# Optimization experiments

Hardware: AMD Instinct MI355X
Metric: run time of the kernel (lower is better)

## Reference

```python
import jax, jax.numpy as jnp
import numpy as np

N_QUBITS = 10
N_QLAYERS = 4
INV_SQRT2 = 1.0 / np.sqrt(2.0)


def setup_inputs() -> dict:
    key = jax.random.key(0)
    k1, k2 = jax.random.split(key)
    x = jax.random.normal(k1, (16, 256, 2 * N_QUBITS), dtype=jnp.float32)
    weights = jax.random.uniform(k2, (N_QLAYERS, N_QUBITS, 3), dtype=jnp.float32,
                                 minval=-np.pi, maxval=np.pi)
    return {"x": x, "weights": weights}


def _ry_mat(t):
    # t: scalar or (B,) -> (...,2,2) complex64 rotation about Y
    c = jnp.cos(t * 0.5)
    s = jnp.sin(t * 0.5)
    row0 = jnp.stack([c, -s], axis=-1)
    row1 = jnp.stack([s, c], axis=-1)
    return jnp.stack([row0, row1], axis=-2).astype(jnp.complex64)


def _rz_mat(p):
    # t: scalar or (B,) -> (...,2,2) complex64 diag(e^{-ip/2}, e^{+ip/2})
    e = jnp.exp(-0.5j * p.astype(jnp.complex64))
    z = jnp.zeros_like(e)
    row0 = jnp.stack([e, z], axis=-1)
    row1 = jnp.stack([z, jnp.conj(e)], axis=-1)
    return jnp.stack([row0, row1], axis=-2)


def _apply_1q(state, U, wire):
    # state: (B, 2,...,2); U: (2,2) shared or (B,2,2) per-sample
    ax = wire + 1
    s = jnp.moveaxis(state, ax, -1)
    if U.ndim == 3:
        s = jnp.einsum('bij,b...j->b...i', U, s)
    else:
        s = jnp.einsum('ij,...j->...i', U, s)
    return jnp.moveaxis(s, -1, ax)


def _apply_cnot(state, ctrl, tgt):
    a, b = ctrl + 1, tgt + 1
    s0 = jax.lax.index_in_dim(state, 0, axis=a, keepdims=True)
    s1 = jax.lax.index_in_dim(state, 1, axis=a, keepdims=True)
    s1 = jnp.flip(s1, axis=b)  # X on target within control=1 block
    return jnp.concatenate([s0, s1], axis=a)


def _circuit(x_flat, weights):
    n = N_QUBITS
    Bf = x_flat.shape[0]
    theta = jnp.pi * (x_flat[:, :n] + 1.0) * 0.5
    phi = jnp.pi * (x_flat[:, n:2 * n] + 1.0) * 0.5
    H = jnp.array([[1.0, 1.0], [1.0, -1.0]], dtype=jnp.complex64) * INV_SQRT2

    # |0...0> batched statevector: (Bf, 2, ..., 2)
    state = jnp.zeros((Bf, 2 ** n), dtype=jnp.complex64).at[:, 0].set(1.0)
    state = state.reshape((Bf,) + (2,) * n)

    # encoding layer
    for i in range(n):
        state = _apply_1q(state, H, i)
        state = _apply_1q(state, _ry_mat(theta[:, i]), i)
        state = _apply_1q(state, _rz_mat(phi[:, i]), i)

    # variational layers
    for layer in range(N_QLAYERS):
        for i in range(n):
            state = _apply_1q(state, _rz_mat(weights[layer, i, 0]), i)
            state = _apply_1q(state, _ry_mat(weights[layer, i, 1]), i)
            state = _apply_1q(state, _rz_mat(weights[layer, i, 2]), i)
        off = 1 if layer % 2 == 0 else n // 2
        for i in range(n):
            state = _apply_cnot(state, i, (i + off) % n)

    # <Z_i> = sum |amp|^2 * (+1 if qubit i = 0 else -1)
    probs = state.real ** 2 + state.imag ** 2
    zs = []
    for i in range(n):
        p = jnp.moveaxis(probs, i + 1, -1).reshape(Bf, -1, 2)
        zs.append(p[..., 0].sum(-1) - p[..., 1].sum(-1))
    return jnp.stack(zs, axis=-1)  # (Bf, n_qubits)


def reference(x, weights):
    B, L, _ = x.shape
    out = _circuit(x.reshape(-1, 2 * N_QUBITS), weights)
    return out.reshape(B, L, N_QUBITS)
```

## Files before the change

### kernel.cpp

```cpp
#include <hip/hip_runtime.h>
#include <math.h>

#define NQ 10
#define NLAYERS 4
#define NGATES (NLAYERS * NQ)

typedef float v2f __attribute__((ext_vector_type(2)));
typedef float v4f __attribute__((ext_vector_type(4)));

__device__ __forceinline__ v2f mk2(float a, float b) { v2f r; r.x = a; r.y = b; return r; }

__device__ __forceinline__ v2f cmul_m(v4f m, v2f s) {
    v2f r = m.xy * s;
    return __builtin_elementwise_fma(m.zw, s.yx, r);
}
__device__ __forceinline__ v2f cfma_m(v2f acc, v4f m, v2f s) {
    acc = __builtin_elementwise_fma(m.xy, s, acc);
    acc = __builtin_elementwise_fma(m.zw, s.yx, acc);
    return acc;
}
__device__ __forceinline__ v2f cmul(v2f a, v2f b) {
    v2f r = a.xx * b;
    return __builtin_elementwise_fma(mk2(-a.y, a.y), b.yx, r);
}
__device__ __forceinline__ v4f pack_u(float re, float im) {
    v4f m; m.x = re; m.y = re; m.z = -im; m.w = im; return m;
}

__host__ __device__ constexpr int pxor1(int v) {
    int y = v; y ^= y >> 1; y ^= y >> 2; y ^= y >> 4; y ^= y >> 8;
    return (y & 0x1FF) | (((y ^ (v >> 9)) & 1) << 9);
}
__host__ __device__ constexpr int pxor5(int v) {
    int lo = v & 31, hi = (v >> 5) & 31;
    return (lo << 5) | (lo ^ hi);
}

__device__ __forceinline__ void apply_gate(v2f* st, const v4f* __restrict__ M, int b) {
    v4f m0 = M[0], m1 = M[1], m2 = M[2], m3 = M[3];
    #pragma unroll
    for (int g = 0; g < 16; ++g) {
        int r0 = ((g >> b) << (b + 1)) | (g & ((1 << b) - 1));
        int r1 = r0 | (1 << b);
        v2f s0v = st[r0], s1v = st[r1];
        v2f n0 = cmul_m(m0, s0v); n0 = cfma_m(n0, m1, s1v);
        v2f n1 = cmul_m(m2, s0v); n1 = cfma_m(n1, m3, s1v);
        st[r0] = n0; st[r1] = n1;
    }
}

__device__ __forceinline__ void load_contig(v2f* st, const v2f* scratch, int lane) {
    const v4f* rp = (const v4f*)(scratch + 34 * lane);
    #pragma unroll
    for (int k = 0; k < 16; ++k) { v4f t = rp[k]; st[2 * k] = t.xy; st[2 * k + 1] = t.zw; }
}

__global__ __launch_bounds__(64) void qsim_kernel(const float* __restrict__ x,
                                                  const float* __restrict__ w,
                                                  float* __restrict__ out)
{
    __shared__ __align__(16) v2f scratch[2176];
    __shared__ __align__(16) v4f matsL[NGATES * 4];
    __shared__ __align__(16) v2f encf[2][NQ][2];

    const int lane = threadIdx.x;
    const int s = lane >> 5, sl = lane & 31;
    const long sample = 2L * blockIdx.x + s;

    if (lane < NGATES) {
        float w0 = w[lane * 3 + 0], w1 = w[lane * 3 + 1], w2 = w[lane * 3 + 2];
        float hs = 0.5f * (w0 + w2), hd = 0.5f * (w0 - w2), hy = 0.5f * w1;
        float cy, sy, cs, ss, cd, sd;
        sincosf(hy, &sy, &cy);
        sincosf(hs, &ss, &cs);
        sincosf(hd, &sd, &cd);
        matsL[lane * 4 + 0] = pack_u( cy * cs, -cy * ss);
        matsL[lane * 4 + 1] = pack_u(-sy * cd, -sy * sd);
        matsL[lane * 4 + 2] = pack_u( sy * cd, -sy * sd);
        matsL[lane * 4 + 3] = pack_u( cy * cs,  cy * ss);
    }
    __syncthreads();

    if (sl < NQ) {
        const float* xs = x + sample * (2 * NQ);
        float th = 0.7853981633974483f * (xs[sl] + 1.0f);
        float ph = 0.7853981633974483f * (xs[NQ + sl] + 1.0f);
        float cy, sy, cp, sp;
        sincosf(th, &sy, &cy);
        sincosf(ph, &sp, &cp);
        const float inv = 0.7071067811865476f;
        float a = (cy - sy) * inv, b = (cy + sy) * inv;
        v2f f0 = mk2(cp * a, -sp * a);
        v2f f1 = mk2(cp * b,  sp * b);
        v4f M0 = matsL[sl * 4 + 0], M1 = matsL[sl * 4 + 1];
        v4f M2 = matsL[sl * 4 + 2], M3 = matsL[sl * 4 + 3];
        encf[s][sl][0] = cfma_m(cmul_m(M0, f0), M1, f1);
        encf[s][sl][1] = cfma_m(cmul_m(M2, f0), M3, f1);
    }
    __syncthreads();

    v2f st[32];
    {
        v2f P = encf[s][5][(sl >> 4) & 1];
        P = cmul(P, encf[s][6][(sl >> 3) & 1]);
        P = cmul(P, encf[s][7][(sl >> 2) & 1]);
        P = cmul(P, encf[s][8][(sl >> 1) & 1]);
        P = cmul(P, encf[s][9][sl & 1]);
        v2f q01[4], q23[4], q234[8], Pq[4];
        #pragma unroll
        for (int a2 = 0; a2 < 4; ++a2) {
            q01[a2] = cmul(encf[s][0][(a2 >> 1) & 1], encf[s][1][a2 & 1]);
            q23[a2] = cmul(encf[s][2][(a2 >> 1) & 1], encf[s][3][a2 & 1]);
        }
        #pragma unroll
        for (int b2 = 0; b2 < 8; ++b2)
            q234[b2] = cmul(q23[b2 >> 1], encf[s][4][b2 & 1]);
        #pragma unroll
        for (int a2 = 0; a2 < 4; ++a2) Pq[a2] = cmul(P, q01[a2]);
        #pragma unroll
        for (int r = 0; r < 32; ++r)
            st[r] = cmul(Pq[r >> 3], q234[r & 7]);
    }

    const int jb1 = pxor1(sl), jb5 = pxor5(sl);

    #pragma unroll
    for (int r = 0; r < 32; ++r) {
        const int j = pxor1(r << 5) ^ jb1;
        scratch[1088 * s + 34 * (j >> 5) + (j & 31)] = st[r];
    }
    __syncthreads();
    load_contig(st, scratch, lane);

    #pragma unroll
    for (int l = 1; l < NLAYERS; ++l) {
        #pragma unroll
        for (int q = 5; q <= 9; ++q)
            apply_gate(st, matsL + (l * NQ + q) * 4, 9 - q);

        __syncthreads();
        {
            v2f* wp = scratch + 1088 * s + sl;
            #pragma unroll
            for (int r = 0; r < 32; ++r) wp[34 * r] = st[r];
        }
        __syncthreads();
        load_contig(st, scratch, lane);

        #pragma unroll
        for (int q = 0; q <= 4; ++q)
            apply_gate(st, matsL + (l * NQ + q) * 4, 4 - q);

        if (l < NLAYERS - 1) {
            __syncthreads();
            #pragma unroll
            for (int r = 0; r < 32; ++r) {
                const int jc = (l & 1) ? pxor5(r << 5) : pxor1(r << 5);
                const int j = jc ^ ((l & 1) ? jb5 : jb1);
                scratch[1088 * s + 34 * (j >> 5) + (j & 31)] = st[r];
            }
            __syncthreads();
            load_contig(st, scratch, lane);
        }
    }

    {
        float p[32];
        #pragma unroll
        for (int r = 0; r < 32; ++r) {
            v2f a = st[r];
            v2f sq = a * a;
            p[r] = sq.x + sq.y;
        }
        float t0 = 0.f, t1 = 0.f, t2 = 0.f, t3 = 0.f, t4 = 0.f;
        float s0a[16], s1a[8], s2a[4], s3a[2];
        #pragma unroll
        for (int k = 0; k < 16; ++k) { s0a[k] = p[2*k] + p[2*k+1]; t0 += p[2*k] - p[2*k+1]; }
        #pragma unroll
        for (int k = 0; k < 8; ++k)  { s1a[k] = s0a[2*k] + s0a[2*k+1]; t1 += s0a[2*k] - s0a[2*k+1]; }
        #pragma unroll
        for (int k = 0; k < 4; ++k)  { s2a[k] = s1a[2*k] + s1a[2*k+1]; t2 += s1a[2*k] - s1a[2*k+1]; }
        #pragma unroll
        for (int k = 0; k < 2; ++k)  { s3a[k] = s2a[2*k] + s2a[2*k+1]; t3 += s2a[2*k] - s2a[2*k+1]; }
        float S = s3a[0] + s3a[1];   t4 = s3a[0] - s3a[1];

        float acc[NQ];
        #pragma unroll
        for (int q = 0; q < 5; ++q)
            acc[q] = ((sl >> (4 - q)) & 1) ? -S : S;
        acc[5] = ((sl >> 4) & 1) ? -t4 : t4;
        acc[6] = ((sl >> 3) & 1) ? -t3 : t3;
        acc[7] = ((sl >> 2) & 1) ? -t2 : t2;
        acc[8] = ((sl >> 1) & 1) ? -t1 : t1;
        acc[9] = (sl & 1)        ? -t0 : t0;

        #pragma unroll
        for (int q = 0; q < NQ; ++q) {
            #pragma unroll
            for (int o = 16; o >= 1; o >>= 1)
                acc[q] += __shfl_xor(acc[q], o);
        }
        float v = acc[0];
        #pragma unroll
        for (int q = 1; q < NQ; ++q) v = (sl == q) ? acc[q] : v;
        if (sl < NQ)
            out[sample * NQ + sl] = v;
    }
}

extern "C" void kernel_launch(void* const* d_in, const int* in_sizes, int n_in,
                              void* d_out, int out_size, void* d_ws, size_t ws_size,
                              hipStream_t stream) {
    const float* x = (const float*)d_in[0];
    const float* w = (const float*)d_in[1];
    float* out = (float*)d_out;
    const int n_samples = in_sizes[0] / (2 * NQ);
    qsim_kernel<<<n_samples / 2, 64, 0, stream>>>(x, w, out);
}
```

Before: 77.23 us.

## Spread each sample's statevector across a full 64-lane wave with shuffle gates

Each block now simulates one sample using all 64 lanes, so each lane holds 16 amplitudes instead of 32 and register pressure drops (launch bounds now request 4 waves). Two qubits per layer are applied through cross-lane shuffles instead of in-register pairs. Unitary storage is halved by exploiting SU(2) structure, the shared-memory transposes use an XOR swizzle instead of padding, and the final reduction becomes a butterfly of Walsh-style shuffles. The cost is more shuffle traffic and twice as many blocks.

Result: slower. 83.28 us (+7.8%).

```diff
diff --git a/kernel.cpp b/kernel.cpp
--- a/kernel.cpp
+++ b/kernel.cpp
@@ -19,6 +19,15 @@
     acc = __builtin_elementwise_fma(m.zw, s.yx, acc);
     return acc;
 }
+__device__ __forceinline__ v2f cmul_mc(v4f m, v2f s) {
+    v2f r = m.xy * s;
+    return __builtin_elementwise_fma(-m.zw, s.yx, r);
+}
+__device__ __forceinline__ v2f cfms_mc(v2f acc, v4f m, v2f s) {
+    acc = __builtin_elementwise_fma(-m.xy, s, acc);
+    acc = __builtin_elementwise_fma(m.zw, s.yx, acc);
+    return acc;
+}
 __device__ __forceinline__ v2f cmul(v2f a, v2f b) {
     v2f r = a.xx * b;
     return __builtin_elementwise_fma(mk2(-a.y, a.y), b.yx, r);
@@ -36,55 +45,73 @@
     return (lo << 5) | (lo ^ hi);
 }
 
-__device__ __forceinline__ void apply_gate(v2f* st, const v4f* __restrict__ M, int b) {
-    v4f m0 = M[0], m1 = M[1], m2 = M[2], m3 = M[3];
-    #pragma unroll
-    for (int g = 0; g < 16; ++g) {
+__device__ __forceinline__ void apply_gate16(v2f* st, const v4f* __restrict__ M, int b) {
+    v4f m0 = M[0], m1 = M[1];
+    #pragma unroll
+    for (int g = 0; g < 8; ++g) {
         int r0 = ((g >> b) << (b + 1)) | (g & ((1 << b) - 1));
         int r1 = r0 | (1 << b);
-        v2f s0v = st[r0], s1v = st[r1];
-        v2f n0 = cmul_m(m0, s0v); n0 = cfma_m(n0, m1, s1v);
-        v2f n1 = cmul_m(m2, s0v); n1 = cfma_m(n1, m3, s1v);
-        st[r0] = n0; st[r1] = n1;
-    }
-}
-
-__device__ __forceinline__ void load_contig(v2f* st, const v2f* scratch, int lane) {
-    const v4f* rp = (const v4f*)(scratch + 34 * lane);
-    #pragma unroll
-    for (int k = 0; k < 16; ++k) { v4f t = rp[k]; st[2 * k] = t.xy; st[2 * k + 1] = t.zw; }
-}
-
-__global__ __launch_bounds__(64) void qsim_kernel(const float* __restrict__ x,
-                                                  const float* __restrict__ w,
-                                                  float* __restrict__ out)
+        v2f s0 = st[r0], s1 = st[r1];
+        st[r0] = cfma_m(cmul_m(m0, s0), m1, s1);
+        st[r1] = cfms_mc(cmul_mc(m0, s1), m1, s0);
+    }
+}
+
+__device__ __forceinline__ v2f shflx2(v2f v, int m) {
+    v2f r;
+    r.x = __shfl_xor(v.x, m, 64);
+    r.y = __shfl_xor(v.y, m, 64);
+    return r;
+}
+
+__device__ __forceinline__ void apply_gate_lane(v2f* st, const v4f* __restrict__ M, int m, int lane) {
+    v4f m0 = M[0], m1 = M[1];
+    v4f mA = m0, mB = m1;
+    if (lane & m) { mA.z = -mA.z; mA.w = -mA.w; mB.x = -mB.x; mB.y = -mB.y; }
+    #pragma unroll
+    for (int r = 0; r < 16; ++r) {
+        v2f mine = st[r];
+        v2f th = shflx2(mine, m);
+        st[r] = cfma_m(cmul_m(mA, mine), mB, th);
+    }
+}
+
+__device__ __forceinline__ void read_row(v2f* st, const v2f* scratch, int lane) {
+    const int e = (lane & 7) << 1;
+    const v2f* row = scratch + lane * 16;
+    #pragma unroll
+    for (int h = 0; h < 8; ++h) {
+        v4f t = *(const v4f*)(row + ((2 * h) ^ e));
+        st[2 * h]     = t.xy;
+        st[2 * h + 1] = t.zw;
+    }
+}
+
+__global__ __launch_bounds__(64, 4) void qsim_kernel(const float* __restrict__ x,
+                                                     const float* __restrict__ w,
+                                                     float* __restrict__ out)
 {
-    __shared__ __align__(16) v2f scratch[2176];
-    __shared__ __align__(16) v4f matsL[NGATES * 4];
-    __shared__ __align__(16) v2f encf[2][NQ][2];
+    __shared__ __align__(16) v2f scratch[1024];
+    __shared__ __align__(16) v4f matsL[NGATES * 2];
+    __shared__ __align__(16) v2f encf[NQ][2];
 
     const int lane = threadIdx.x;
-    const int s = lane >> 5, sl = lane & 31;
-    const long sample = 2L * blockIdx.x + s;
+    const long sample = blockIdx.x;
 
     if (lane < NGATES) {
-        float w0 = w[lane * 3 + 0], w1 = w[lane * 3 + 1], w2 = w[lane * 3 + 2];
-        float hs = 0.5f * (w0 + w2), hd = 0.5f * (w0 - w2), hy = 0.5f * w1;
+        float w0 = w[lane*3+0], w1 = w[lane*3+1], w2 = w[lane*3+2];
+        float hs = 0.5f*(w0+w2), hd = 0.5f*(w0-w2), hy = 0.5f*w1;
         float cy, sy, cs, ss, cd, sd;
         sincosf(hy, &sy, &cy);
         sincosf(hs, &ss, &cs);
         sincosf(hd, &sd, &cd);
-        matsL[lane * 4 + 0] = pack_u( cy * cs, -cy * ss);
-        matsL[lane * 4 + 1] = pack_u(-sy * cd, -sy * sd);
-        matsL[lane * 4 + 2] = pack_u( sy * cd, -sy * sd);
-        matsL[lane * 4 + 3] = pack_u( cy * cs,  cy * ss);
-    }
-    __syncthreads();
-
-    if (sl < NQ) {
+        matsL[lane*2+0] = pack_u( cy*cs, -cy*ss);
+        matsL[lane*2+1] = pack_u(-sy*cd, -sy*sd);
+    }
+    if (lane < NQ) {
         const float* xs = x + sample * (2 * NQ);
-        float th = 0.7853981633974483f * (xs[sl] + 1.0f);
-        float ph = 0.7853981633974483f * (xs[NQ + sl] + 1.0f);
+        float th = 0.7853981633974483f * (xs[lane] + 1.0f);
+        float ph = 0.7853981633974483f * (xs[NQ + lane] + 1.0f);
         float cy, sy, cp, sp;
         sincosf(th, &sy, &cy);
         sincosf(ph, &sp, &cp);
@@ -92,119 +119,121 @@
         float a = (cy - sy) * inv, b = (cy + sy) * inv;
         v2f f0 = mk2(cp * a, -sp * a);
         v2f f1 = mk2(cp * b,  sp * b);
-        v4f M0 = matsL[sl * 4 + 0], M1 = matsL[sl * 4 + 1];
-        v4f M2 = matsL[sl * 4 + 2], M3 = matsL[sl * 4 + 3];
-        encf[s][sl][0] = cfma_m(cmul_m(M0, f0), M1, f1);
-        encf[s][sl][1] = cfma_m(cmul_m(M2, f0), M3, f1);
+        v4f M0 = matsL[lane*2+0], M1 = matsL[lane*2+1];
+        encf[lane][0] = cfma_m(cmul_m(M0, f0), M1, f1);
+        encf[lane][1] = cfms_mc(cmul_mc(M0, f1), M1, f0);
     }
     __syncthreads();
 
-    v2f st[32];
+    v2f st[16];
     {
-        v2f P = encf[s][5][(sl >> 4) & 1];
-        P = cmul(P, encf[s][6][(sl >> 3) & 1]);
-        P = cmul(P, encf[s][7][(sl >> 2) & 1]);
-        P = cmul(P, encf[s][8][(sl >> 1) & 1]);
-        P = cmul(P, encf[s][9][sl & 1]);
-        v2f q01[4], q23[4], q234[8], Pq[4];
+        v2f L = cmul(encf[4][(lane >> 5) & 1], encf[5][(lane >> 4) & 1]);
+        L = cmul(L, encf[6][(lane >> 3) & 1]);
+        L = cmul(L, encf[7][(lane >> 2) & 1]);
+        L = cmul(L, encf[8][(lane >> 1) & 1]);
+        L = cmul(L, encf[9][lane & 1]);
+        v2f hi2[4], lo2[4], Lh[4];
         #pragma unroll
         for (int a2 = 0; a2 < 4; ++a2) {
-            q01[a2] = cmul(encf[s][0][(a2 >> 1) & 1], encf[s][1][a2 & 1]);
-            q23[a2] = cmul(encf[s][2][(a2 >> 1) & 1], encf[s][3][a2 & 1]);
-        }
-        #pragma unroll
-        for (int b2 = 0; b2 < 8; ++b2)
-            q234[b2] = cmul(q23[b2 >> 1], encf[s][4][b2 & 1]);
-        #pragma unroll
-        for (int a2 = 0; a2 < 4; ++a2) Pq[a2] = cmul(P, q01[a2]);
-        #pragma unroll
-        for (int r = 0; r < 32; ++r)
-            st[r] = cmul(Pq[r >> 3], q234[r & 7]);
-    }
-
-    const int jb1 = pxor1(sl), jb5 = pxor5(sl);
-
-    #pragma unroll
-    for (int r = 0; r < 32; ++r) {
-        const int j = pxor1(r << 5) ^ jb1;
-        scratch[1088 * s + 34 * (j >> 5) + (j & 31)] = st[r];
-    }
+            hi2[a2] = cmul(encf[0][(a2 >> 1) & 1], encf[1][a2 & 1]);
+            lo2[a2] = cmul(encf[2][(a2 >> 1) & 1], encf[3][a2 & 1]);
+        }
+        #pragma unroll
+        for (int a2 = 0; a2 < 4; ++a2) Lh[a2] = cmul(L, hi2[a2]);
+        #pragma unroll
+        for (int r = 0; r < 16; ++r)
+            st[r] = cmul(Lh[r >> 2], lo2[r & 3]);
+    }
+
+    const int jb1 = pxor1(lane), jb5 = pxor5(lane);
+
     __syncthreads();
-    load_contig(st, scratch, lane);
+    #pragma unroll
+    for (int r = 0; r < 16; ++r) {
+        const int jc = pxor1(r << 6);
+        const int jp = jc ^ jb1;
+        const int row = jp >> 4;
+        scratch[(row << 4) + ((jp & 15) ^ ((row & 7) << 1))] = st[r];
+    }
+    __syncthreads();
+    read_row(st, scratch, lane);
 
     #pragma unroll
     for (int l = 1; l < NLAYERS; ++l) {
-        #pragma unroll
-        for (int q = 5; q <= 9; ++q)
-            apply_gate(st, matsL + (l * NQ + q) * 4, 9 - q);
+        const v4f* Ml = matsL + l * NQ * 2;
+        apply_gate16(st, Ml + 6*2, 3);
+        apply_gate16(st, Ml + 7*2, 2);
+        apply_gate16(st, Ml + 8*2, 1);
+        apply_gate16(st, Ml + 9*2, 0);
+        apply_gate_lane(st, Ml + 4*2, 2, lane);
+        apply_gate_lane(st, Ml + 5*2, 1, lane);
 
         __syncthreads();
         {
-            v2f* wp = scratch + 1088 * s + sl;
+            const int b0 = (lane & 3) << 8;
+            const int cc = lane >> 2;
             #pragma unroll
-            for (int r = 0; r < 32; ++r) wp[34 * r] = st[r];
+            for (int r = 0; r < 16; ++r)
+                scratch[b0 + (r << 4) + (cc ^ ((r & 7) << 1))] = st[r];
         }
         __syncthreads();
-        load_contig(st, scratch, lane);
-
-        #pragma unroll
-        for (int q = 0; q <= 4; ++q)
-            apply_gate(st, matsL + (l * NQ + q) * 4, 4 - q);
+        read_row(st, scratch, lane);
+
+        apply_gate16(st, Ml + 0*2, 3);
+        apply_gate16(st, Ml + 1*2, 2);
+        apply_gate16(st, Ml + 2*2, 1);
+        apply_gate16(st, Ml + 3*2, 0);
 
         if (l < NLAYERS - 1) {
             __syncthreads();
+            const int jb = (l & 1) ? jb5 : jb1;
             #pragma unroll
-            for (int r = 0; r < 32; ++r) {
-                const int jc = (l & 1) ? pxor5(r << 5) : pxor1(r << 5);
-                const int j = jc ^ ((l & 1) ? jb5 : jb1);
-                scratch[1088 * s + 34 * (j >> 5) + (j & 31)] = st[r];
+            for (int r = 0; r < 16; ++r) {
+                const int jc = (l & 1) ? pxor5(r << 6) : pxor1(r << 6);
+                const int jp = jc ^ jb;
+                const int row = jp >> 4;
+                scratch[(row << 4) + ((jp & 15) ^ ((row & 7) << 1))] = st[r];
             }
             __syncthreads();
-            load_contig(st, scratch, lane);
+            read_row(st, scratch, lane);
         }
     }
 
     {
-        float p[32];
-        #pragma unroll
-        for (int r = 0; r < 32; ++r) {
-            v2f a = st[r];
-            v2f sq = a * a;
-            p[r] = sq.x + sq.y;
-        }
-        float t0 = 0.f, t1 = 0.f, t2 = 0.f, t3 = 0.f, t4 = 0.f;
-        float s0a[16], s1a[8], s2a[4], s3a[2];
-        #pragma unroll
-        for (int k = 0; k < 16; ++k) { s0a[k] = p[2*k] + p[2*k+1]; t0 += p[2*k] - p[2*k+1]; }
-        #pragma unroll
-        for (int k = 0; k < 8; ++k)  { s1a[k] = s0a[2*k] + s0a[2*k+1]; t1 += s0a[2*k] - s0a[2*k+1]; }
-        #pragma unroll
-        for (int k = 0; k < 4; ++k)  { s2a[k] = s1a[2*k] + s1a[2*k+1]; t2 += s1a[2*k] - s1a[2*k+1]; }
-        #pragma unroll
-        for (int k = 0; k < 2; ++k)  { s3a[k] = s2a[2*k] + s2a[2*k+1]; t3 += s2a[2*k] - s2a[2*k+1]; }
-        float S = s3a[0] + s3a[1];   t4 = s3a[0] - s3a[1];
-
-        float acc[NQ];
-        #pragma unroll
-        for (int q = 0; q < 5; ++q)
-            acc[q] = ((sl >> (4 - q)) & 1) ? -S : S;
-        acc[5] = ((sl >> 4) & 1) ? -t4 : t4;
-        acc[6] = ((sl >> 3) & 1) ? -t3 : t3;
-        acc[7] = ((sl >> 2) & 1) ? -t2 : t2;
-        acc[8] = ((sl >> 1) & 1) ? -t1 : t1;
-        acc[9] = (sl & 1)        ? -t0 : t0;
-
-        #pragma unroll
-        for (int q = 0; q < NQ; ++q) {
-            #pragma unroll
-            for (int o = 16; o >= 1; o >>= 1)
-                acc[q] += __shfl_xor(acc[q], o);
-        }
-        float v = acc[0];
-        #pragma unroll
-        for (int q = 1; q < NQ; ++q) v = (sl == q) ? acc[q] : v;
-        if (sl < NQ)
-            out[sample * NQ + sl] = v;
+        float p[16];
+        #pragma unroll
+        for (int r = 0; r < 16; ++r) {
+            v2f a = st[r]; v2f q2 = a * a; p[r] = q2.x + q2.y;
+        }
+        float s0[8], s1[4], s2[2];
+        float tb0 = 0.f, tb1 = 0.f, tb2, tb3, S;
+        #pragma unroll
+        for (int k = 0; k < 8; ++k) { s0[k] = p[2*k] + p[2*k+1]; tb0 += p[2*k] - p[2*k+1]; }
+        #pragma unroll
+        for (int k = 0; k < 4; ++k) { s1[k] = s0[2*k] + s0[2*k+1]; tb1 += s0[2*k] - s0[2*k+1]; }
+        #pragma unroll
+        for (int k = 0; k < 2; ++k) { s2[k] = s1[2*k] + s1[2*k+1]; }
+        tb2 = (s1[0] - s1[1]) + (s1[2] - s1[3]);
+        S   = s2[0] + s2[1];
+        tb3 = s2[0] - s2[1];
+
+        float wS = S, w0t = tb0, w1t = tb1, w2t = tb2, w3t = tb3;
+        #pragma unroll
+        for (int m = 1; m < 64; m <<= 1) {
+            float t;
+            t = __shfl_xor(wS,  m, 64); wS  = (lane & m) ? (t - wS)  : (wS  + t);
+            t = __shfl_xor(w0t, m, 64); w0t = (lane & m) ? (t - w0t) : (w0t + t);
+            t = __shfl_xor(w1t, m, 64); w1t = (lane & m) ? (t - w1t) : (w1t + t);
+            t = __shfl_xor(w2t, m, 64); w2t = (lane & m) ? (t - w2t) : (w2t + t);
+            t = __shfl_xor(w3t, m, 64); w3t = (lane & m) ? (t - w3t) : (w3t + t);
+        }
+        float* ob = out + sample * NQ;
+        if (lane == 16)      { ob[0] = wS; ob[5] = w3t; }
+        else if (lane == 8)  { ob[1] = wS; ob[6] = w2t; }
+        else if (lane == 4)  { ob[2] = wS; ob[7] = w1t; }
+        else if (lane == 2)  { ob[3] = wS; ob[8] = w0t; }
+        else if (lane == 1)  { ob[4] = wS; }
+        else if (lane == 33) { ob[9] = wS; }
     }
 }
 
@@ -215,5 +244,5 @@
     const float* w = (const float*)d_in[1];
     float* out = (float*)d_out;
     const int n_samples = in_sizes[0] / (2 * NQ);
-    qsim_kernel<<<n_samples / 2, 64, 0, stream>>>(x, w, out);
-}
+    qsim_kernel<<<n_samples, 64, 0, stream>>>(x, w, out);
+}
```

## Build initial state directly in permuted layout and compress gate matrices

Applied to the files above, without the earlier changes.

Builds the product-state encoding directly in the register layout that follows the first CNOT permutation, which removes one LDS write/sync/read round trip. Each SU(2) gate is now stored as a single v4f (a, b) instead of four packed v4f, which cuts LDS reads per gate, and the packed-vector complex math is replaced with scalar fmaf chains. The risk is a change in instruction count and VALU packing, since scalar fma may not use the v_pk_fma path.

Result: slower. 84.81 us (+9.8%).

```diff
diff --git a/kernel.cpp b/kernel.cpp
--- a/kernel.cpp
+++ b/kernel.cpp
@@ -10,21 +10,18 @@
 
 __device__ __forceinline__ v2f mk2(float a, float b) { v2f r; r.x = a; r.y = b; return r; }
 
-__device__ __forceinline__ v2f cmul_m(v4f m, v2f s) {
-    v2f r = m.xy * s;
-    return __builtin_elementwise_fma(m.zw, s.yx, r);
-}
-__device__ __forceinline__ v2f cfma_m(v2f acc, v4f m, v2f s) {
-    acc = __builtin_elementwise_fma(m.xy, s, acc);
-    acc = __builtin_elementwise_fma(m.zw, s.yx, acc);
-    return acc;
-}
-__device__ __forceinline__ v2f cmul(v2f a, v2f b) {
-    v2f r = a.xx * b;
-    return __builtin_elementwise_fma(mk2(-a.y, a.y), b.yx, r);
-}
-__device__ __forceinline__ v4f pack_u(float re, float im) {
-    v4f m; m.x = re; m.y = re; m.z = -im; m.w = im; return m;
+__device__ __forceinline__ v2f cmulS(v2f a, v2f b) {
+    return mk2(fmaf(a.x, b.x, -(a.y * b.y)), fmaf(a.x, b.y, a.y * b.x));
+}
+__device__ __forceinline__ v2f grow0(v4f m, v2f s0, v2f s1) {
+    float re = fmaf(m.x, s0.x, fmaf(-m.y, s0.y, fmaf(m.z, s1.x, -(m.w * s1.y))));
+    float im = fmaf(m.x, s0.y, fmaf( m.y, s0.x, fmaf(m.z, s1.y,   m.w * s1.x)));
+    return mk2(re, im);
+}
+__device__ __forceinline__ v2f grow1(v4f m, v2f s0, v2f s1) {
+    float re = fmaf(-m.z, s0.x, fmaf(-m.w, s0.y, fmaf(m.x, s1.x,   m.y * s1.y)));
+    float im = fmaf( m.w, s0.x, fmaf(-m.z, s0.y, fmaf(m.x, s1.y, -(m.y * s1.x))));
+    return mk2(re, im);
 }
 
 __host__ __device__ constexpr int pxor1(int v) {
@@ -36,16 +33,14 @@
     return (lo << 5) | (lo ^ hi);
 }
 
-__device__ __forceinline__ void apply_gate(v2f* st, const v4f* __restrict__ M, int b) {
-    v4f m0 = M[0], m1 = M[1], m2 = M[2], m3 = M[3];
+__device__ __forceinline__ void apply_gate(v2f* st, v4f m, int b) {
     #pragma unroll
     for (int g = 0; g < 16; ++g) {
         int r0 = ((g >> b) << (b + 1)) | (g & ((1 << b) - 1));
         int r1 = r0 | (1 << b);
-        v2f s0v = st[r0], s1v = st[r1];
-        v2f n0 = cmul_m(m0, s0v); n0 = cfma_m(n0, m1, s1v);
-        v2f n1 = cmul_m(m2, s0v); n1 = cfma_m(n1, m3, s1v);
-        st[r0] = n0; st[r1] = n1;
+        v2f s0 = st[r0], s1 = st[r1];
+        st[r0] = grow0(m, s0, s1);
+        st[r1] = grow1(m, s0, s1);
     }
 }
 
@@ -60,7 +55,7 @@
                                                   float* __restrict__ out)
 {
     __shared__ __align__(16) v2f scratch[2176];
-    __shared__ __align__(16) v4f matsL[NGATES * 4];
+    __shared__ __align__(16) v4f matsL[NGATES];
     __shared__ __align__(16) v2f encf[2][NQ][2];
 
     const int lane = threadIdx.x;
@@ -74,10 +69,8 @@
         sincosf(hy, &sy, &cy);
         sincosf(hs, &ss, &cs);
         sincosf(hd, &sd, &cd);
-        matsL[lane * 4 + 0] = pack_u( cy * cs, -cy * ss);
-        matsL[lane * 4 + 1] = pack_u(-sy * cd, -sy * sd);
-        matsL[lane * 4 + 2] = pack_u( sy * cd, -sy * sd);
-        matsL[lane * 4 + 3] = pack_u( cy * cs,  cy * ss);
+        v4f m; m.x = cy * cs; m.y = -cy * ss; m.z = -sy * cd; m.w = -sy * sd;
+        matsL[lane] = m;
     }
     __syncthreads();
 
@@ -92,51 +85,49 @@
         float a = (cy - sy) * inv, b = (cy + sy) * inv;
         v2f f0 = mk2(cp * a, -sp * a);
         v2f f1 = mk2(cp * b,  sp * b);
-        v4f M0 = matsL[sl * 4 + 0], M1 = matsL[sl * 4 + 1];
-        v4f M2 = matsL[sl * 4 + 2], M3 = matsL[sl * 4 + 3];
-        encf[s][sl][0] = cfma_m(cmul_m(M0, f0), M1, f1);
-        encf[s][sl][1] = cfma_m(cmul_m(M2, f0), M3, f1);
+        v4f m = matsL[sl];
+        encf[s][sl][0] = grow0(m, f0, f1);
+        encf[s][sl][1] = grow1(m, f0, f1);
     }
     __syncthreads();
 
     v2f st[32];
     {
-        v2f P = encf[s][5][(sl >> 4) & 1];
-        P = cmul(P, encf[s][6][(sl >> 3) & 1]);
-        P = cmul(P, encf[s][7][(sl >> 2) & 1]);
-        P = cmul(P, encf[s][8][(sl >> 1) & 1]);
-        P = cmul(P, encf[s][9][sl & 1]);
-        v2f q01[4], q23[4], q234[8], Pq[4];
-        #pragma unroll
-        for (int a2 = 0; a2 < 4; ++a2) {
-            q01[a2] = cmul(encf[s][0][(a2 >> 1) & 1], encf[s][1][a2 & 1]);
-            q23[a2] = cmul(encf[s][2][(a2 >> 1) & 1], encf[s][3][a2 & 1]);
-        }
-        #pragma unroll
-        for (int b2 = 0; b2 < 8; ++b2)
-            q234[b2] = cmul(q23[b2 >> 1], encf[s][4][b2 & 1]);
-        #pragma unroll
-        for (int a2 = 0; a2 < 4; ++a2) Pq[a2] = cmul(P, q01[a2]);
-        #pragma unroll
-        for (int r = 0; r < 32; ++r)
-            st[r] = cmul(Pq[r >> 3], q234[r & 7]);
+        v2f Lc = cmulS(encf[s][2][((sl >> 2) ^ (sl >> 3)) & 1],
+                 cmulS(encf[s][3][((sl >> 1) ^ (sl >> 2)) & 1],
+                       encf[s][4][(sl ^ (sl >> 1)) & 1]));
+        v2f g5s0 = encf[s][5][sl & 1];
+        v2f g5s1 = encf[s][5][(sl & 1) ^ 1];
+        const int l4 = (sl >> 4) & 1, l34 = ((sl >> 3) ^ (sl >> 4)) & 1;
+        v2f h0 = cmulS(encf[s][0][l4],     encf[s][1][l34]);
+        v2f h1 = cmulS(encf[s][0][l4 ^ 1], encf[s][1][l34 ^ 1]);
+        v2f k4[4];
+        k4[0] = cmulS(encf[s][9][0], h0);
+        k4[1] = cmulS(encf[s][9][1], h1);
+        k4[2] = cmulS(encf[s][9][1], h0);
+        k4[3] = cmulS(encf[s][9][0], h1);
+        v2f Av[2], Bv[4], Cv[8], Dv[16];
+        Av[0] = cmulS(Lc, g5s0); Av[1] = cmulS(Lc, g5s1);
+        #pragma unroll
+        for (int i = 0; i < 4; ++i)  Bv[i] = cmulS(Av[i >> 1], encf[s][6][((i >> 1) ^ i) & 1]);
+        #pragma unroll
+        for (int i = 0; i < 8; ++i)  Cv[i] = cmulS(Bv[i >> 1], encf[s][7][((i >> 1) ^ i) & 1]);
+        #pragma unroll
+        for (int i = 0; i < 16; ++i) Dv[i] = cmulS(Cv[i >> 1], encf[s][8][((i >> 1) ^ i) & 1]);
+        #pragma unroll
+        for (int r = 0; r < 32; ++r) st[r] = cmulS(Dv[r >> 1], k4[r & 3]);
     }
 
     const int jb1 = pxor1(sl), jb5 = pxor5(sl);
-
-    #pragma unroll
-    for (int r = 0; r < 32; ++r) {
-        const int j = pxor1(r << 5) ^ jb1;
-        scratch[1088 * s + 34 * (j >> 5) + (j & 31)] = st[r];
-    }
-    __syncthreads();
-    load_contig(st, scratch, lane);
 
     #pragma unroll
     for (int l = 1; l < NLAYERS; ++l) {
-        #pragma unroll
-        for (int q = 5; q <= 9; ++q)
-            apply_gate(st, matsL + (l * NQ + q) * 4, 9 - q);
+        const v4f* Ml = matsL + l * NQ;
+        apply_gate(st, Ml[5], 4);
+        apply_gate(st, Ml[6], 3);
+        apply_gate(st, Ml[7], 2);
+        apply_gate(st, Ml[8], 1);
+        apply_gate(st, Ml[9], 0);
 
         __syncthreads();
         {
@@ -147,9 +138,11 @@
         __syncthreads();
         load_contig(st, scratch, lane);
 
-        #pragma unroll
-        for (int q = 0; q <= 4; ++q)
-            apply_gate(st, matsL + (l * NQ + q) * 4, 4 - q);
+        apply_gate(st, Ml[0], 4);
+        apply_gate(st, Ml[1], 3);
+        apply_gate(st, Ml[2], 2);
+        apply_gate(st, Ml[3], 1);
+        apply_gate(st, Ml[4], 0);
 
         if (l < NLAYERS - 1) {
             __syncthreads();
@@ -169,8 +162,7 @@
         #pragma unroll
         for (int r = 0; r < 32; ++r) {
             v2f a = st[r];
-            v2f sq = a * a;
-            p[r] = sq.x + sq.y;
+            p[r] = fmaf(a.x, a.x, a.y * a.y);
         }
         float t0 = 0.f, t1 = 0.f, t2 = 0.f, t3 = 0.f, t4 = 0.f;
         float s0a[16], s1a[8], s2a[4], s3a[2];
```
